# Kernel optimization log

Hardware: AMD Instinct MI355X
Metric: run time of the kernel (lower is better)

The kernel has to match this reference:

```python
import jax, jax.numpy as jnp
import numpy as np

B, L, E, H = 1, 4096, 1024, 16
D = E // H
EPS = 1e-6


def setup_inputs() -> dict:
    key = jax.random.key(0)
    k1, k2, k3 = jax.random.split(key, 3)
    # fan-in scaled init to keep activations sane
    x = jax.random.normal(k1, (B, L, E), dtype=jnp.float32)
    qkv_w = jax.random.normal(k2, (E, 3 * E), dtype=jnp.float32) / np.sqrt(E)
    qkv_b = jnp.zeros((3 * E,), dtype=jnp.float32)
    out_w = jax.random.normal(k3, (E, E), dtype=jnp.float32) / np.sqrt(E)
    out_b = jnp.zeros((E,), dtype=jnp.float32)
    return {"x": x, "qkv_w": qkv_w, "qkv_b": qkv_b, "out_w": out_w, "out_b": out_b}


def reference(x, qkv_w, qkv_b, out_w, out_b):
    b, l, e = x.shape
    qkv = x @ qkv_w + qkv_b                      # (B, L, 3E)
    q, k, v = jnp.split(qkv, 3, axis=-1)
    # (B, L, E) -> (B, H, L, D)
    q = q.reshape(b, l, H, D).transpose(0, 2, 1, 3)
    k = k.reshape(b, l, H, D).transpose(0, 2, 1, 3)
    v = v.reshape(b, l, H, D).transpose(0, 2, 1, 3)
    q_prime = jax.nn.elu(q) + 1.0
    k_prime = jax.nn.elu(k) + 1.0
    # cumulative sum of per-position outer products k'_l v_l^T : (B,H,L,D,D)
    kv_prod = jnp.einsum('bhld,bhle->bhlde', k_prime, v)
    kv_cumsum = jnp.cumsum(kv_prod, axis=2)
    context = jnp.einsum('bhld,bhlde->bhle', q_prime, kv_cumsum)  # (B,H,L,D)
    k_cumsum = jnp.cumsum(k_prime, axis=2)                        # (B,H,L,D)
    norm = jnp.einsum('bhld,bhld->bhl', q_prime, k_cumsum)        # (B,H,L)
    output = context / (norm[..., None] + EPS)
    output = output.transpose(0, 2, 1, 3).reshape(b, l, e)
    return output @ out_w + out_b
```

## Files before the change

### kernel.cpp

```cpp
#include <hip/hip_runtime.h>
#include <cstddef>
#include <cstdint>

#define L_SEQ 4096
#define EMB   1024
#define NH    16
#define HD    64
#define N3    3072
#define CHUNK 64
#define NCHUNK 64
#define EPS 1e-6f

typedef __attribute__((ext_vector_type(8))) short   bf16x8;
typedef __attribute__((ext_vector_type(4))) short   bf16x4;
typedef __attribute__((ext_vector_type(4))) float   floatx4;

#define AS1 __attribute__((address_space(1)))
#define AS3 __attribute__((address_space(3)))

__device__ __forceinline__ void gload_lds16(const void* g, void* l) {
    __builtin_amdgcn_global_load_lds((AS1 const unsigned int*)g,
                                     (AS3 unsigned int*)l, 16, 0, 0);
}

__device__ __forceinline__ short f2bf(float f) {
    union { float f; unsigned u; } a; a.f = f;
    unsigned r = a.u + 0x7fffu + ((a.u >> 16) & 1u);
    return (short)(r >> 16);
}
__device__ __forceinline__ float bf2f(short s) {
    union { unsigned u; float f; } a; a.u = ((unsigned)(unsigned short)s) << 16;
    return a.f;
}

__device__ __forceinline__ void transpose_tile(const float* __restrict__ W,
                                               short* __restrict__ WT,
                                               int K, int N, int bx, int by,
                                               float (*t)[65], int tid)
{
    const int r  = tid >> 4;
    const int c4 = (tid & 15) << 2;
#pragma unroll
    for (int s = 0; s < 4; ++s) {
        const int k = r + s * 16;
        const floatx4 v = *(const floatx4*)&W[(size_t)(by * 64 + k) * N + bx * 64 + c4];
        t[k][c4 + 0] = v[0]; t[k][c4 + 1] = v[1];
        t[k][c4 + 2] = v[2]; t[k][c4 + 3] = v[3];
    }
    __syncthreads();
#pragma unroll
    for (int s = 0; s < 4; ++s) {
        const int n = r + s * 16;
        bf16x4 o;
        o[0] = f2bf(t[c4 + 0][n]); o[1] = f2bf(t[c4 + 1][n]);
        o[2] = f2bf(t[c4 + 2][n]); o[3] = f2bf(t[c4 + 3][n]);
        *(bf16x4*)&WT[(size_t)(bx * 64 + n) * K + by * 64 + c4] = o;
    }
}

__global__ __launch_bounds__(256)
void prep(const float* __restrict__ x, short* __restrict__ xb,
          const float* __restrict__ qkv_w, short* __restrict__ qwt,
          const float* __restrict__ out_w, short* __restrict__ owt)
{
    __shared__ float t[64][65];
    const int b = blockIdx.x;
    const int tid = threadIdx.x;
    if (b < 2048) {
        const int i = b * 256 + tid;
        const floatx4 a = *(const floatx4*)(x + (size_t)i * 8);
        const floatx4 c = *(const floatx4*)(x + (size_t)i * 8 + 4);
        bf16x8 o;
        o[0] = f2bf(a[0]); o[1] = f2bf(a[1]); o[2] = f2bf(a[2]); o[3] = f2bf(a[3]);
        o[4] = f2bf(c[0]); o[5] = f2bf(c[1]); o[6] = f2bf(c[2]); o[7] = f2bf(c[3]);
        *(bf16x8*)(xb + (size_t)i * 8) = o;
    } else if (b < 2048 + 768) {
        const int u = b - 2048;
        transpose_tile(qkv_w, qwt, EMB, N3, u % 48, u / 48, t, tid);
    } else {
        const int u = b - 2816;
        transpose_tile(out_w, owt, EMB, EMB, u & 15, u >> 4, t, tid);
    }
}

#define MFMA16 __builtin_amdgcn_mfma_f32_16x16x32_bf16

__global__ __launch_bounds__(512, 2)
void mfma_gemm_qkv256(const short* __restrict__ A, const short* __restrict__ BT,
                      const float* __restrict__ bias,
                      short* __restrict__ OQ, short* __restrict__ OK,
                      short* __restrict__ OV)
{
    __shared__ __align__(16) short lds[57344];
    const int tid  = threadIdx.x;
    const int lane = tid & 63;
    const int wave = tid >> 6;
    const int wr   = wave >> 2;
    const int wc   = wave & 3;
    const int frow = lane & 15;
    const int quad = lane >> 4;
    const int q8   = quad * 8;
    const int bx = blockIdx.x;
    const int by = blockIdx.y;

    const short* Ab = A  + (size_t)(by * 256) * 1024;
    const short* Bb = BT + (size_t)(bx * 192) * 1024;

    const int trow = tid >> 3;
    const int ccol = (tid & 7) * 8;
    const int scol = ccol ^ ((trow & 14) << 2);
    const int sx   = (frow & 14) << 2;
    const int wcb  = wc * 48 + frow;

#define STG_A(LBASE, GPTR) do {                                             \
        const short* g_ = (GPTR);                                           \
        _Pragma("unroll")                                                   \
        for (int j_ = 0; j_ < 2; ++j_) {                                    \
            const int r_ = j_ * 64 + trow;                                  \
            gload_lds16(g_ + (size_t)r_ * 1024 + scol,                      \
                        &lds[(LBASE) + r_ * 64 + ccol]);                    \
        }                                                                   \
    } while (0)

#define STG_B(LBASE, GPTR) do {                                             \
        const short* g_ = (GPTR);                                           \
        _Pragma("unroll")                                                   \
        for (int j_ = 0; j_ < 3; ++j_) {                                    \
            const int r_ = j_ * 64 + trow;                                  \
            gload_lds16(g_ + (size_t)r_ * 1024 + scol,                      \
                        &lds[(LBASE) + r_ * 64 + ccol]);                    \
        }                                                                   \
    } while (0)

#define LDA(BASE, R, KS) \
    (*(const bf16x8*)&lds[(BASE) + (R) * 64 + ((((KS) * 32) + q8) ^ sx)])

    floatx4 acc[8][3] = {};
    bf16x8  bq[3][2];

#define PHASE(ABASE, BBASE, QD, RDB, VM, ...) do {                          \
        const int Rr_ = wr * 128 + (QD) * 32 + frow;                        \
        bf16x8 a0_ = LDA((ABASE), Rr_,      0);                             \
        bf16x8 a1_ = LDA((ABASE), Rr_,      1);                             \
        bf16x8 a2_ = LDA((ABASE), Rr_ + 16, 0);                             \
        bf16x8 a3_ = LDA((ABASE), Rr_ + 16, 1);                             \
        if (RDB) {                                                          \
            _Pragma("unroll")                                               \
            for (int ni_ = 0; ni_ < 3; ++ni_) {                             \
                bq[ni_][0] = LDA((BBASE), wcb + ni_ * 16, 0);               \
                bq[ni_][1] = LDA((BBASE), wcb + ni_ * 16, 1);               \
            }                                                               \
        }                                                                   \
        __VA_ARGS__;                                                        \
        __builtin_amdgcn_sched_barrier(0);                                  \
        __builtin_amdgcn_s_barrier();                                       \
        asm volatile("s_waitcnt lgkmcnt(0)" ::: "memory");                  \
        __builtin_amdgcn_sched_barrier(0);                                  \
        __builtin_amdgcn_s_setprio(1);                                      \
        _Pragma("unroll")                                                   \
        for (int ni_ = 0; ni_ < 3; ++ni_) {                                 \
            acc[2*(QD)  ][ni_] = MFMA16(a0_, bq[ni_][0], acc[2*(QD)  ][ni_], 0,0,0); \
            acc[2*(QD)  ][ni_] = MFMA16(a1_, bq[ni_][1], acc[2*(QD)  ][ni_], 0,0,0); \
            acc[2*(QD)+1][ni_] = MFMA16(a2_, bq[ni_][0], acc[2*(QD)+1][ni_], 0,0,0); \
            acc[2*(QD)+1][ni_] = MFMA16(a3_, bq[ni_][1], acc[2*(QD)+1][ni_], 0,0,0); \
        }                                                                   \
        __builtin_amdgcn_s_setprio(0);                                      \
        if (VM) asm volatile("s_waitcnt vmcnt(3)" ::: "memory");            \
        __builtin_amdgcn_s_barrier();                                       \
        __builtin_amdgcn_sched_barrier(0);                                  \
    } while (0)

    STG_A(0,     Ab);
    STG_A(8192,  Ab + 131072);
    STG_B(16384, Bb);
    STG_B(45056, Bb + 64);
    asm volatile("s_waitcnt vmcnt(3)" ::: "memory");
    __builtin_amdgcn_s_barrier();
    __builtin_amdgcn_sched_barrier(0);

#pragma unroll 1
    for (int it = 0; it < 8; ++it) {
        const int k1  = (2 * it + 1) * 64;
        const int kn0 = ((2 * it + 2) & 15) * 64;
        const int kn1 = ((2 * it + 3) & 15) * 64;

        PHASE(0, 16384, 0, 1, 0,
              STG_A(28672, Ab + k1); STG_A(36864, Ab + 131072 + k1));
        PHASE(0, 16384, 1, 0, 0, STG_B(16384, Bb + kn0));
        PHASE(0, 16384, 2, 0, 0, ((void)0));
        PHASE(0, 16384, 3, 0, 1, ((void)0));
        PHASE(28672, 45056, 0, 1, 0, STG_A(0, Ab + kn0));
        PHASE(28672, 45056, 1, 0, 0, STG_A(8192, Ab + 131072 + kn0));
        PHASE(28672, 45056, 2, 0, 0, STG_B(45056, Bb + kn1));
        PHASE(28672, 45056, 3, 0, 1, ((void)0));
    }

    __syncthreads();

    const int wbase = wave * 6144;
    const int colg0 = bx * 192 + wc * 48;
    const int L0 = by * 256 + wr * 128;
#pragma unroll
    for (int ni = 0; ni < 3; ++ni) {
        const int n = colg0 + ni * 16 + frow;
        const float bv = bias[n];
        const bool do_elu = (n >> 10) < 2;
#pragma unroll
        for (int mi = 0; mi < 8; ++mi)
#pragma unroll
            for (int r = 0; r < 4; ++r) {
                float v = acc[mi][ni][r] + bv;
                if (do_elu) v = (v > 0.f) ? (v + 1.f) : __expf(v);
                lds[wbase + (mi * 16 + quad * 4 + r) * 48 + ni * 16 + frow] = f2bf(v);
            }
    }
#pragma unroll
    for (int s = 0; s < 12; ++s) {
        const int chunk = s * 64 + lane;
        const int row = chunk / 6, cc = (chunk % 6) * 8;
        const bf16x8 val = *(const bf16x8*)&lds[wbase + row * 48 + cc];
        const int n0 = colg0 + cc;
        const int rsel = n0 >> 10;
        const int h = (n0 & 1023) >> 6;
        const int d = n0 & 63;
        short* base = (rsel == 0) ? OQ : (rsel == 1 ? OK : OV);
        *(bf16x8*)&base[((size_t)(h * L_SEQ + L0 + row)) * HD + d] = val;
    }
#undef PHASE
#undef LDA
#undef STG_A
#undef STG_B
}

__global__ __launch_bounds__(256)
void mfma_gemm_out(const short* __restrict__ A, const short* __restrict__ BT,
                   const float* __restrict__ bias, float* __restrict__ OF,
                   int N, int K)
{
    __shared__ __align__(16) short smem[12288];
    short* pan[4] = { smem, smem + 2048, smem + 6144, smem + 8192 };
    const int tid  = threadIdx.x;
    const int lane = tid & 63;
    const int wave = tid >> 6;
    const int wm = (wave >> 1) * 32;
    const int wn = (wave & 1) * 64;
    const int bx = blockIdx.x;
    const int by = blockIdx.y;
    const int frow = lane & 15;
    const int quad = lane >> 4;
    const int fko  = quad << 3;

    const short* Ab = A  + (size_t)(by * 64) * K;
    const short* Bb = BT + (size_t)(bx * 128) * K;

    floatx4 acc[2][4] = {};

    for (int k0 = 0; k0 < K; k0 += 64) {
#pragma unroll
        for (int p = 0; p < 2; ++p) {
            const int kp = k0 + p * 32;
            {
                const int row = tid >> 2;
                const int kc  = (tid & 3) << 3;
                gload_lds16(Ab + (size_t)row * K + kp + kc, &pan[p * 2 + 0][tid << 3]);
            }
#pragma unroll
            for (int q = 0; q < 2; ++q) {
                const int ib = q * 256 + tid;
                const int row = ib >> 2;
                const int kc  = (ib & 3) << 3;
                gload_lds16(Bb + (size_t)row * K + kp + kc, &pan[p * 2 + 1][ib << 3]);
            }
        }
        __syncthreads();
#pragma unroll
        for (int p = 0; p < 2; ++p) {
            bf16x8 af[2], bfv[4];
#pragma unroll
            for (int mi = 0; mi < 2; ++mi)
                af[mi] = *(const bf16x8*)&pan[p * 2 + 0][(wm + mi * 16 + frow) * 32 + fko];
#pragma unroll
            for (int ni = 0; ni < 4; ++ni)
                bfv[ni] = *(const bf16x8*)&pan[p * 2 + 1][(wn + ni * 16 + frow) * 32 + fko];
#pragma unroll
            for (int mi = 0; mi < 2; ++mi)
#pragma unroll
                for (int ni = 0; ni < 4; ++ni)
                    acc[mi][ni] = __builtin_amdgcn_mfma_f32_16x16x32_bf16(
                        af[mi], bfv[ni], acc[mi][ni], 0, 0, 0);
        }
        __syncthreads();
    }

    const int rq = quad << 2;
#pragma unroll
    for (int ni = 0; ni < 4; ++ni) {
        const int n = bx * 128 + wn + ni * 16 + frow;
        const float bv = bias[n];
#pragma unroll
        for (int mi = 0; mi < 2; ++mi)
#pragma unroll
            for (int r = 0; r < 4; ++r) {
                const int m = by * 64 + wm + mi * 16 + rq + r;
                OF[(size_t)m * N + n] = acc[mi][ni][r] + bv;
            }
    }
}

#define SP 72

__global__ __launch_bounds__(256, 4)
void chunk_state(const short* __restrict__ Kb, const short* __restrict__ Vb,
                 short* __restrict__ ScTb, float* __restrict__ zc)
{
    __shared__ __align__(16) short Vt[64 * SP];
    __shared__ __align__(16) short Kt[64 * SP];
    const int c = blockIdx.x, h = blockIdx.y;
    const int tid = threadIdx.x, lane = tid & 63, wave = tid >> 6;
    const int frow = lane & 15;
    const int quad = lane >> 4;
    const int fko  = quad << 3;
    const int wm   = wave << 4;
    const short* Kg = Kb + ((size_t)h * L_SEQ + (size_t)c * CHUNK) * HD;
    const short* Vg = Vb + ((size_t)h * L_SEQ + (size_t)c * CHUNK) * HD;

#pragma unroll
    for (int q = 0; q < 2; ++q) {
        const int idx = q * 256 + tid;
        const int l = idx >> 3, c8 = (idx & 7) << 3;
        const bf16x8 vv = *(const bf16x8*)&Vg[l * 64 + c8];
        const bf16x8 kk = *(const bf16x8*)&Kg[l * 64 + c8];
#pragma unroll
        for (int j = 0; j < 8; ++j) {
            Vt[(c8 + j) * SP + l] = vv[j];
            Kt[(c8 + j) * SP + l] = kk[j];
        }
    }
    __syncthreads();

    const bf16x8 af0 = *(const bf16x8*)&Vt[(wm + frow) * SP + fko];
    const bf16x8 af1 = *(const bf16x8*)&Vt[(wm + frow) * SP + 32 + fko];

    floatx4 acc[4] = {};
#pragma unroll
    for (int n = 0; n < 4; ++n) {
        const bf16x8 kf0 = *(const bf16x8*)&Kt[(n * 16 + frow) * SP + fko];
        const bf16x8 kf1 = *(const bf16x8*)&Kt[(n * 16 + frow) * SP + 32 + fko];
        acc[n] = MFMA16(af0, kf0, acc[n], 0, 0, 0);
        acc[n] = MFMA16(af1, kf1, acc[n], 0, 0, 0);
    }

    short* Sout = ScTb + (size_t)(h * NCHUNK + c) * 4096;
#pragma unroll
    for (int n = 0; n < 4; ++n)
#pragma unroll
        for (int r = 0; r < 4; ++r) {
            const int e = wm + quad * 4 + r;
            const int d = n * 16 + frow;
            Sout[e * 64 + d] = f2bf(acc[n][r]);
        }

    if (wave == 0) {
        bf16x8 ones;
#pragma unroll
        for (int j = 0; j < 8; ++j) ones[j] = (short)0x3F80;
        floatx4 zacc[4] = {};
#pragma unroll
        for (int n = 0; n < 4; ++n) {
            const bf16x8 kf0 = *(const bf16x8*)&Kt[(n * 16 + frow) * SP + fko];
            const bf16x8 kf1 = *(const bf16x8*)&Kt[(n * 16 + frow) * SP + 32 + fko];
            zacc[n] = MFMA16(ones, kf0, zacc[n], 0, 0, 0);
            zacc[n] = MFMA16(ones, kf1, zacc[n], 0, 0, 0);
        }
        if (quad == 0) {
#pragma unroll
            for (int n = 0; n < 4; ++n)
                zc[(size_t)(h * NCHUNK + c) * 64 + n * 16 + frow] = zacc[n][0];
        }
    }
}

__global__ __launch_bounds__(256)
void prefix_scan(const short* __restrict__ ScTb, const float* __restrict__ zc,
                 short* __restrict__ S0b)
{
    const int g = blockIdx.x * 256 + threadIdx.x;
    const int h  = g >> 12;
    const int ed = g & 4095;
    const int e  = ed >> 6;
    const int d  = ed & 63;
    const short* src = ScTb + (size_t)h * NCHUNK * 4096 + ed;
    float run = 0.f;
    for (int cb = 0; cb < NCHUNK; cb += 8) {
        short v[8];
#pragma unroll
        for (int u = 0; u < 8; ++u) v[u] = src[(size_t)(cb + u) * 4096];
#pragma unroll
        for (int u = 0; u < 8; ++u) {
            S0b[((size_t)((h * NCHUNK + cb + u) * 65 + e)) * 64 + d] = f2bf(run);
            run += bf2f(v[u]);
        }
    }
    if (g < NH * HD) {
        const int h2 = g >> 6, d2 = g & 63;
        float rz = 0.f;
        for (int cb = 0; cb < NCHUNK; cb += 8) {
            float w[8];
#pragma unroll
            for (int u = 0; u < 8; ++u)
                w[u] = zc[((size_t)(h2 * NCHUNK + cb + u)) * HD + d2];
#pragma unroll
            for (int u = 0; u < 8; ++u) {
                S0b[((size_t)((h2 * NCHUNK + cb + u) * 65 + 64)) * 64 + d2] = f2bf(rz);
                rz += w[u];
            }
        }
    }
}

__global__ __launch_bounds__(256)
void chunk_attn(const short* __restrict__ Qb, const short* __restrict__ Kb,
                const short* __restrict__ Vb, const short* __restrict__ S0b,
                short* __restrict__ attn)
{
    __shared__ __align__(16) short Vs[65 * SP];
    __shared__ __align__(16) short Ks[64 * SP];
    __shared__ __align__(16) short Qs[64 * SP];
    __shared__ __align__(16) short As[64 * SP];
    const int c = blockIdx.x, h = blockIdx.y;
    const int tid = threadIdx.x, lane = tid & 63, wave = tid >> 6;
    const size_t rb = ((size_t)h * L_SEQ + (size_t)c * CHUNK) * HD;
    const short* Qg = Qb + rb;
    const short* Kg = Kb + rb;
    const short* Vg = Vb + rb;
    const short* Sg = S0b + (size_t)(h * NCHUNK + c) * 65 * 64;

#pragma unroll
    for (int q = 0; q < 2; ++q) {
        const int idx = q * 256 + tid;
        const int row = idx >> 3, c8 = (idx & 7) << 3;
        const bf16x8 vv = *(const bf16x8*)&Vg[row * 64 + c8];
        const bf16x8 kk = *(const bf16x8*)&Kg[row * 64 + c8];
        const bf16x8 qq = *(const bf16x8*)&Qg[row * 64 + c8];
#pragma unroll
        for (int j = 0; j < 8; ++j) Vs[(c8 + j) * SP + row] = vv[j];
        *(bf16x8*)&Ks[row * SP + c8] = kk;
        *(bf16x8*)&Qs[row * SP + c8] = qq;
    }
    if (tid < 64) Vs[64 * SP + tid] = (short)0x3F80;
    __syncthreads();

    const int frow = lane & 15;
    const int quad = lane >> 4;
    const int fko  = quad << 3;
    const int wm   = wave << 4;

    const bf16x8 qf0 = *(const bf16x8*)&Qs[(wm + frow) * SP + fko];
    const bf16x8 qf1 = *(const bf16x8*)&Qs[(wm + frow) * SP + 32 + fko];

    floatx4 sacc[4] = {};
#pragma unroll
    for (int n = 0; n < 4; ++n) {
        const bf16x8 kf0 = *(const bf16x8*)&Ks[(n * 16 + frow) * SP + fko];
        const bf16x8 kf1 = *(const bf16x8*)&Ks[(n * 16 + frow) * SP + 32 + fko];
        sacc[n] = MFMA16(qf0, kf0, sacc[n], 0, 0, 0);
        sacc[n] = MFMA16(qf1, kf1, sacc[n], 0, 0, 0);
    }
#pragma unroll
    for (int n = 0; n < 4; ++n)
#pragma unroll
        for (int r = 0; r < 4; ++r) {
            const int i = wm + quad * 4 + r;
            const int j = n * 16 + frow;
            As[i * SP + j] = (j <= i) ? f2bf(sacc[n][r]) : (short)0;
        }
    const bf16x8 af0 = *(const bf16x8*)&As[(wm + frow) * SP + fko];
    const bf16x8 af1 = *(const bf16x8*)&As[(wm + frow) * SP + 32 + fko];

    floatx4 oacc[5] = {};
#pragma unroll
    for (int n = 0; n < 4; ++n) {
        const bf16x8 vf0 = *(const bf16x8*)&Vs[(n * 16 + frow) * SP + fko];
        const bf16x8 vf1 = *(const bf16x8*)&Vs[(n * 16 + frow) * SP + 32 + fko];
        oacc[n] = MFMA16(af0, vf0, oacc[n], 0, 0, 0);
        oacc[n] = MFMA16(af1, vf1, oacc[n], 0, 0, 0);
        const bf16x8 sf0 = *(const bf16x8*)&Sg[(n * 16 + frow) * 64 + fko];
        const bf16x8 sf1 = *(const bf16x8*)&Sg[(n * 16 + frow) * 64 + 32 + fko];
        oacc[n] = MFMA16(qf0, sf0, oacc[n], 0, 0, 0);
        oacc[n] = MFMA16(qf1, sf1, oacc[n], 0, 0, 0);
    }
    {
        const bf16x8 vf0 = *(const bf16x8*)&Vs[64 * SP + fko];
        const bf16x8 vf1 = *(const bf16x8*)&Vs[64 * SP + 32 + fko];
        oacc[4] = MFMA16(af0, vf0, oacc[4], 0, 0, 0);
        oacc[4] = MFMA16(af1, vf1, oacc[4], 0, 0, 0);
        const bf16x8 sf0 = *(const bf16x8*)&Sg[64 * 64 + fko];
        const bf16x8 sf1 = *(const bf16x8*)&Sg[64 * 64 + 32 + fko];
        oacc[4] = MFMA16(qf0, sf0, oacc[4], 0, 0, 0);
        oacc[4] = MFMA16(qf1, sf1, oacc[4], 0, 0, 0);
    }
#pragma unroll
    for (int r = 0; r < 4; ++r) {
        const float norm = __shfl(oacc[4][r], lane & 48) + EPS;
        const float inv = 1.f / norm;
        const int i = wm + quad * 4 + r;
#pragma unroll
        for (int n = 0; n < 4; ++n)
            As[i * SP + n * 16 + frow] = f2bf(oacc[n][r] * inv);
    }
    __syncthreads();
#pragma unroll
    for (int t = 0; t < 2; ++t) {
        const int idx = t * 256 + tid;
        const int row = idx >> 3, c8 = (idx & 7) << 3;
        *(bf16x8*)&attn[(size_t)(c * CHUNK + row) * EMB + h * HD + c8] =
            *(const bf16x8*)&As[row * SP + c8];
    }
}

extern "C" void kernel_launch(void* const* d_in, const int* in_sizes, int n_in,
                              void* d_out, int out_size, void* d_ws, size_t ws_size,
                              hipStream_t stream)
{
    const float* x     = (const float*)d_in[0];
    const float* qkv_w = (const float*)d_in[1];
    const float* qkv_b = (const float*)d_in[2];
    const float* out_w = (const float*)d_in[3];
    const float* out_b = (const float*)d_in[4];
    float* out = (float*)d_out;

    short* ws    = (short*)d_ws;
    short* Qb    = ws;
    short* Kb    = Qb + 4194304;
    short* Vb    = Kb + 4194304;
    short* xb    = Vb + 4194304;
    short* qwt   = xb + 4194304;
    short* owt   = qwt + 3145728;
    short* attnb = owt + 1048576;
    short* ScTb  = attnb + 4194304;
    short* S0b   = ScTb + 4194304;
    float* zc    = (float*)(S0b + 4259840);

    prep<<<dim3(3072), 256, 0, stream>>>(x, xb, qkv_w, qwt, out_w, owt);
    mfma_gemm_qkv256<<<dim3(N3 / 192, L_SEQ / 256), 512, 0, stream>>>(
        xb, qwt, qkv_b, Qb, Kb, Vb);
    chunk_state<<<dim3(NCHUNK, NH), 256, 0, stream>>>(Kb, Vb, ScTb, zc);
    prefix_scan<<<dim3((NH * 4096) / 256), 256, 0, stream>>>(ScTb, zc, S0b);
    chunk_attn<<<dim3(NCHUNK, NH), 256, 0, stream>>>(Qb, Kb, Vb, S0b, attnb);
    mfma_gemm_out<<<dim3(EMB / 128, L_SEQ / 64), 256, 0, stream>>>(
        attnb, owt, out_b, out, EMB, EMB);
}
```

Measured before the change: 158.9 us.

## Swizzle block order for L2 locality, XOR-swizzle LDS in out GEMM, deepen scan batching

Both GEMM kernels remap the block index so that consecutive workgroups share A/B panels (grouped rasterization for L2 reuse). The output-projection GEMM now loads full 64-wide K tiles into LDS with an XOR swizzle, so fragment reads avoid bank conflicts, and it drops the split two-panel layout. The prefix scan batches 16 chunk loads instead of 8 to expose more memory-level parallelism. The cost is more registers per thread in the scan, and the new block remaps assume fixed grid dimensions.

```diff
diff --git a/kernel.cpp b/kernel.cpp
--- a/kernel.cpp
+++ b/kernel.cpp
@@ -100,8 +100,10 @@
     const int frow = lane & 15;
     const int quad = lane >> 4;
     const int q8   = quad * 8;
-    const int bx = blockIdx.x;
-    const int by = blockIdx.y;
+    const int fid = blockIdx.y * 16 + blockIdx.x;
+    const int nf  = (fid & 7) * 32 + (fid >> 3);
+    const int bx  = nf & 15;
+    const int by  = nf >> 4;
 
     const short* Ab = A  + (size_t)(by * 256) * 1024;
     const short* Bb = BT + (size_t)(bx * 192) * 1024;
@@ -238,17 +240,19 @@
                    int N, int K)
 {
     __shared__ __align__(16) short smem[12288];
-    short* pan[4] = { smem, smem + 2048, smem + 6144, smem + 8192 };
     const int tid  = threadIdx.x;
     const int lane = tid & 63;
     const int wave = tid >> 6;
     const int wm = (wave >> 1) * 32;
     const int wn = (wave & 1) * 64;
-    const int bx = blockIdx.x;
-    const int by = blockIdx.y;
+    const int fid = blockIdx.y * 8 + blockIdx.x;
+    const int nf  = (fid & 7) * 64 + (fid >> 3);
+    const int bx  = nf & 7;
+    const int by  = nf >> 3;
     const int frow = lane & 15;
     const int quad = lane >> 4;
-    const int fko  = quad << 3;
+    const int q8   = quad << 3;
+    const int sx   = (frow & 14) << 2;
 
     const short* Ab = A  + (size_t)(by * 64) * K;
     const short* Bb = BT + (size_t)(bx * 128) * K;
@@ -257,38 +261,42 @@
 
     for (int k0 = 0; k0 < K; k0 += 64) {
 #pragma unroll
-        for (int p = 0; p < 2; ++p) {
-            const int kp = k0 + p * 32;
-            {
-                const int row = tid >> 2;
-                const int kc  = (tid & 3) << 3;
-                gload_lds16(Ab + (size_t)row * K + kp + kc, &pan[p * 2 + 0][tid << 3]);
+        for (int q = 0; q < 2; ++q) {
+            const int idx = q * 256 + tid;
+            const int row = idx >> 3;
+            const int c8  = (idx & 7) << 3;
+            gload_lds16(Ab + (size_t)row * K + k0 + (c8 ^ ((row & 14) << 2)),
+                        &smem[idx << 3]);
+        }
+#pragma unroll
+        for (int q = 0; q < 4; ++q) {
+            const int idx = q * 256 + tid;
+            const int row = idx >> 3;
+            const int c8  = (idx & 7) << 3;
+            gload_lds16(Bb + (size_t)row * K + k0 + (c8 ^ ((row & 14) << 2)),
+                        &smem[4096 + (idx << 3)]);
+        }
+        __syncthreads();
+        bf16x8 af[2][2], bfv[4][2];
+#pragma unroll
+        for (int mi = 0; mi < 2; ++mi)
+#pragma unroll
+            for (int ks = 0; ks < 2; ++ks)
+                af[mi][ks] = *(const bf16x8*)
+                    &smem[(wm + mi * 16 + frow) * 64 + ((ks * 32 + q8) ^ sx)];
+#pragma unroll
+        for (int ni = 0; ni < 4; ++ni)
+#pragma unroll
+            for (int ks = 0; ks < 2; ++ks)
+                bfv[ni][ks] = *(const bf16x8*)
+                    &smem[4096 + (wn + ni * 16 + frow) * 64 + ((ks * 32 + q8) ^ sx)];
+#pragma unroll
+        for (int mi = 0; mi < 2; ++mi)
+#pragma unroll
+            for (int ni = 0; ni < 4; ++ni) {
+                acc[mi][ni] = MFMA16(af[mi][0], bfv[ni][0], acc[mi][ni], 0, 0, 0);
+                acc[mi][ni] = MFMA16(af[mi][1], bfv[ni][1], acc[mi][ni], 0, 0, 0);
             }
-#pragma unroll
-            for (int q = 0; q < 2; ++q) {
-                const int ib = q * 256 + tid;
-                const int row = ib >> 2;
-                const int kc  = (ib & 3) << 3;
-                gload_lds16(Bb + (size_t)row * K + kp + kc, &pan[p * 2 + 1][ib << 3]);
-            }
-        }
-        __syncthreads();
-#pragma unroll
-        for (int p = 0; p < 2; ++p) {
-            bf16x8 af[2], bfv[4];
-#pragma unroll
-            for (int mi = 0; mi < 2; ++mi)
-                af[mi] = *(const bf16x8*)&pan[p * 2 + 0][(wm + mi * 16 + frow) * 32 + fko];
-#pragma unroll
-            for (int ni = 0; ni < 4; ++ni)
-                bfv[ni] = *(const bf16x8*)&pan[p * 2 + 1][(wn + ni * 16 + frow) * 32 + fko];
-#pragma unroll
-            for (int mi = 0; mi < 2; ++mi)
-#pragma unroll
-                for (int ni = 0; ni < 4; ++ni)
-                    acc[mi][ni] = __builtin_amdgcn_mfma_f32_16x16x32_bf16(
-                        af[mi], bfv[ni], acc[mi][ni], 0, 0, 0);
-        }
         __syncthreads();
     }
 
@@ -391,12 +399,12 @@
     const int d  = ed & 63;
     const short* src = ScTb + (size_t)h * NCHUNK * 4096 + ed;
     float run = 0.f;
-    for (int cb = 0; cb < NCHUNK; cb += 8) {
-        short v[8];
-#pragma unroll
-        for (int u = 0; u < 8; ++u) v[u] = src[(size_t)(cb + u) * 4096];
-#pragma unroll
-        for (int u = 0; u < 8; ++u) {
+    for (int cb = 0; cb < NCHUNK; cb += 16) {
+        short v[16];
+#pragma unroll
+        for (int u = 0; u < 16; ++u) v[u] = src[(size_t)(cb + u) * 4096];
+#pragma unroll
+        for (int u = 0; u < 16; ++u) {
             S0b[((size_t)((h * NCHUNK + cb + u) * 65 + e)) * 64 + d] = f2bf(run);
             run += bf2f(v[u]);
         }
@@ -404,13 +412,13 @@
     if (g < NH * HD) {
         const int h2 = g >> 6, d2 = g & 63;
         float rz = 0.f;
-        for (int cb = 0; cb < NCHUNK; cb += 8) {
-            float w[8];
-#pragma unroll
-            for (int u = 0; u < 8; ++u)
+        for (int cb = 0; cb < NCHUNK; cb += 16) {
+            float w[16];
+#pragma unroll
+            for (int u = 0; u < 16; ++u)
                 w[u] = zc[((size_t)(h2 * NCHUNK + cb + u)) * HD + d2];
 #pragma unroll
-            for (int u = 0; u < 8; ++u) {
+            for (int u = 0; u < 16; ++u) {
                 S0b[((size_t)((h2 * NCHUNK + cb + u) * 65 + 64)) * 64 + d2] = f2bf(rz);
                 rz += w[u];
             }
```

New measurement: 156.3 us. About the same (-1.7%).
